# Kernel tuning notes

Measured on AMD Instinct MI355X. Metric: run time of the kernel, lower is better.

Reference implementation:

```python
import jax, jax.numpy as jnp
import numpy as np

HID, INTER, DK = 768, 1536, 128
NEG_INF = 1.0e12
LOG512 = float(np.log(512.0))


def setup_inputs() -> dict:
    key = jax.random.key(0)
    k1, k2, k3 = jax.random.split(key, 3)
    B, S = 4, 2048
    hidden_states = jax.random.normal(k1, (B, S, HID), dtype=jnp.float32)
    attention_mask = jnp.ones((B, S), dtype=jnp.int32)
    # i_dense: hidden -> 2*INTER + DK (no bias); o_dense: INTER -> hidden (no bias)
    Wi = jax.random.normal(k2, (HID, 2 * INTER + DK), dtype=jnp.float32) * (HID ** -0.5)
    Wo = jax.random.normal(k3, (INTER, HID), dtype=jnp.float32) * (INTER ** -0.5)
    q_gamma = jnp.ones((DK,), dtype=jnp.float32)  # ScaleOffset scale, offset=False
    k_gamma = jnp.ones((DK,), dtype=jnp.float32)
    return {"hidden_states": hidden_states, "Wi": Wi, "Wo": Wo,
            "q_gamma": q_gamma, "k_gamma": k_gamma,
            "attention_mask": attention_mask}


def reference(hidden_states, Wi, Wo, q_gamma, k_gamma, attention_mask):
    # i_dense + swish, then split into u, v, qk
    x = jax.nn.silu(jnp.einsum('bsh,ho->bso', hidden_states, Wi))
    u = x[..., :INTER]
    v = x[..., INTER:2 * INTER]
    qk = x[..., 2 * INTER:]
    q = qk * q_gamma
    k = qk * k_gamma
    # single-head attention scores
    a = jnp.einsum('bmd,bnd->bmn', q, k) / (DK ** 0.5)
    mask = attention_mask[:, None, :]  # [B,1,N]
    a = jnp.where(mask == 0, -NEG_INF, a)
    l = jnp.sum(attention_mask, axis=-1, keepdims=True)[:, :, None].astype(a.dtype)  # [B,1,1]
    # softmax_plus: softmax(a * log(l) / log(512))
    A = jax.nn.softmax(a * jnp.log(l) / LOG512, axis=-1)
    # dropout inactive in eval mode
    o = jnp.einsum('bmi,ih->bmh', u * jnp.einsum('bmn,bnd->bmd', A, v), Wo)
    return o
```

## Files before the change

### kernel.cpp

```cpp
#include <hip/hip_runtime.h>
#include <hip/hip_bf16.h>
#include <math.h>

#define BATCH 4
#define SEQ   2048
#define HID   768
#define INTER 1536
#define DK    128
#define NTOT  3200
#define MROWS 8192
#define LN512 6.2383246250395075f

typedef _Float16 half8  __attribute__((ext_vector_type(8)));
typedef float    floatx4 __attribute__((ext_vector_type(4)));

typedef const __attribute__((address_space(1))) unsigned int* gas1_t;
typedef __attribute__((address_space(3))) unsigned int* las3_t;

static __device__ __forceinline__ void load16(const _Float16* g, _Float16* l) {
    __builtin_amdgcn_global_load_lds((gas1_t)g, (las3_t)l, 16, 0, 0);
}
#define WAIT_VM(N)    asm volatile("s_waitcnt vmcnt(" #N ")" ::: "memory")
#define WAIT_LGKM0()  asm volatile("s_waitcnt lgkmcnt(0)" ::: "memory")
#define BARRIER_RAW() asm volatile("s_barrier" ::: "memory")

__global__ void cast_h_kernel(const float* __restrict__ in, _Float16* __restrict__ out, int n) {
    int i = (blockIdx.x * blockDim.x + threadIdx.x) * 8;
    if (i < n) {
        float4 a = *reinterpret_cast<const float4*>(in + i);
        float4 b = *reinterpret_cast<const float4*>(in + i + 4);
        half8 h = {(_Float16)a.x, (_Float16)a.y, (_Float16)a.z, (_Float16)a.w,
                   (_Float16)b.x, (_Float16)b.y, (_Float16)b.z, (_Float16)b.w};
        *reinterpret_cast<half8*>(out + i) = h;
    }
}

__global__ void trans_wi_kernel(const float* __restrict__ Wi, _Float16* __restrict__ WiT) {
    __shared__ _Float16 tile[32][33];
    const int c0 = blockIdx.x * 32, r0 = blockIdx.y * 32;
    const int tx = threadIdx.x, ty = threadIdx.y;
#pragma unroll
    for (int j = 0; j < 32; j += 8)
        tile[tx][ty + j] = (_Float16)Wi[(size_t)(r0 + ty + j) * NTOT + c0 + tx];
    __syncthreads();
#pragma unroll
    for (int j = 0; j < 32; j += 8)
        WiT[(size_t)(c0 + ty + j) * HID + r0 + tx] = tile[ty + j][tx];
}

__global__ void trans_wo_kernel(const float* __restrict__ Wo, _Float16* __restrict__ WoT) {
    __shared__ _Float16 tile[32][33];
    const int c0 = blockIdx.x * 32, r0 = blockIdx.y * 32;
    const int tx = threadIdx.x, ty = threadIdx.y;
#pragma unroll
    for (int j = 0; j < 32; j += 8)
        tile[tx][ty + j] = (_Float16)Wo[(size_t)(r0 + ty + j) * HID + c0 + tx];
    __syncthreads();
#pragma unroll
    for (int j = 0; j < 32; j += 8)
        WoT[(size_t)(c0 + ty + j) * INTER + r0 + tx] = tile[ty + j][tx];
}

__global__ void mask_scales_kernel(const int* __restrict__ mask, float* __restrict__ scales) {
    __shared__ int sh[256];
    int b = blockIdx.x;
    int s = 0;
    for (int i = threadIdx.x; i < SEQ; i += 256) s += mask[b * SEQ + i];
    sh[threadIdx.x] = s;
    __syncthreads();
    for (int off = 128; off > 0; off >>= 1) {
        if (threadIdx.x < off) sh[threadIdx.x] += sh[threadIdx.x + off];
        __syncthreads();
    }
    if (threadIdx.x == 0) scales[b] = logf((float)sh[0]) / LN512;
}

struct TileCtx {
    int tid, wave, lane, quad, l16, wm, wn, c0, c1, sw;
};
static __device__ __forceinline__ TileCtx make_ctx() {
    TileCtx t;
    t.tid = threadIdx.x;
    t.wave = t.tid >> 6; t.lane = t.tid & 63;
    t.quad = t.lane >> 4; t.l16 = t.lane & 15;
    t.wm = (t.wave & 1) * 64;
    t.wn = (t.wave >> 1) * 64;
    t.c0 = t.tid;
    t.c1 = t.tid + 256;
    t.sw = (t.l16 >> 1) & 3;
    return t;
}

static __device__ __forceinline__ void gemm_mainloop_db(
    const TileCtx& t,
    const _Float16* __restrict__ Ag, int lda,
    const _Float16* __restrict__ Bg, int ldb,
    int K, _Float16* smem, floatx4 acc[4][4])
{
    const int ar0 = t.c0 >> 2, ak0 = ((t.c0 & 3) ^ ((t.c0 >> 3) & 3)) * 8;
    const int ar1 = t.c1 >> 2, ak1 = ((t.c1 & 3) ^ ((t.c1 >> 3) & 3)) * 8;
    const _Float16* a0 = Ag + (size_t)ar0 * lda + ak0;
    const _Float16* a1 = Ag + (size_t)ar1 * lda + ak1;
    const _Float16* b0 = Bg + (size_t)ar0 * ldb + ak0;
    const _Float16* b1 = Bg + (size_t)ar1 * ldb + ak1;
    _Float16* Asl = smem + t.c0 * 8;
    _Float16* Bsl = smem + 8192 + t.c0 * 8;

    const int qsw = (t.quad ^ t.sw) * 8;

    load16(a0, Asl);
    load16(a1, Asl + 2048);
    load16(b0, Bsl);
    load16(b1, Bsl + 2048);

    int buf = 0;
    for (int k0 = 0; k0 < K; k0 += 32) {
        if (k0 + 32 < K) {
            const int nb = (buf ^ 1) * 4096;
            load16(a0 + k0 + 32, Asl + nb);
            load16(a1 + k0 + 32, Asl + nb + 2048);
            load16(b0 + k0 + 32, Bsl + nb);
            load16(b1 + k0 + 32, Bsl + nb + 2048);
            WAIT_VM(4);
        } else {
            WAIT_VM(0);
        }
        BARRIER_RAW();
        const _Float16* Ab = smem + buf * 4096;
        const _Float16* Bb = smem + 8192 + buf * 4096;
        half8 af[4], bf[4];
#pragma unroll
        for (int mt = 0; mt < 4; ++mt)
            af[mt] = *reinterpret_cast<const half8*>(Ab + (t.wm + mt * 16 + t.l16) * 32 + qsw);
#pragma unroll
        for (int nt = 0; nt < 4; ++nt)
            bf[nt] = *reinterpret_cast<const half8*>(Bb + (t.wn + nt * 16 + t.l16) * 32 + qsw);
#pragma unroll
        for (int mt = 0; mt < 4; ++mt)
#pragma unroll
            for (int nt = 0; nt < 4; ++nt)
                acc[mt][nt] = __builtin_amdgcn_mfma_f32_16x16x32_f16(af[mt], bf[nt], acc[mt][nt], 0, 0, 0);
        WAIT_LGKM0();
        BARRIER_RAW();
        buf ^= 1;
    }
}

__global__ __launch_bounds__(256) void gemm1_kernel(
    const _Float16* __restrict__ Hb, const _Float16* __restrict__ WiT,
    const float* __restrict__ qg, const float* __restrict__ kg,
    _Float16* __restrict__ u, _Float16* __restrict__ vT,
    _Float16* __restrict__ q, _Float16* __restrict__ k)
{
    __shared__ _Float16 smem[16384];
    TileCtx t = make_ctx();
    const int f = blockIdx.x;
    const int xcd = f & 7, i = f >> 3;
    const int m0 = ((xcd << 3) | (i & 7)) * 128;
    const int n0 = (i >> 3) * 128;

    floatx4 acc[4][4] = {};
    gemm_mainloop_db(t, Hb + (size_t)m0 * HID, HID, WiT + (size_t)n0 * HID, HID, HID, smem, acc);

    if (n0 >= INTER && n0 < 2 * INTER) {
        const int bb = m0 >> 11, sloc = m0 & (SEQ - 1), cI = n0 - INTER;
#pragma unroll
        for (int mt = 0; mt < 4; ++mt) {
#pragma unroll
            for (int nt = 0; nt < 4; ++nt) {
                int c = t.wn + nt * 16 + t.l16;
#pragma unroll
                for (int i2 = 0; i2 < 4; ++i2) {
                    int r = t.wm + mt * 16 + t.quad * 4 + i2;
                    float x = acc[mt][nt][i2];
                    float y = x / (1.0f + __expf(-x));
                    smem[c * 128 + (r ^ ((c & 15) << 3))] = (_Float16)y;
                }
            }
        }
        __syncthreads();
#pragma unroll
        for (int p = 0; p < 8; ++p) {
            int chunk = t.tid + p * 256;
            int cl = chunk >> 4, sc = chunk & 15;
            int scs = sc ^ (cl & 15);
            half8 v = *reinterpret_cast<const half8*>(smem + cl * 128 + scs * 8);
            *reinterpret_cast<half8*>(vT + ((size_t)bb * INTER + cI + cl) * SEQ + sloc + sc * 8) = v;
        }
    } else {
#pragma unroll
        for (int mt = 0; mt < 4; ++mt) {
#pragma unroll
            for (int nt = 0; nt < 4; ++nt) {
                int col = n0 + t.wn + nt * 16 + t.l16;
#pragma unroll
                for (int i2 = 0; i2 < 4; ++i2) {
                    int row = m0 + t.wm + mt * 16 + t.quad * 4 + i2;
                    float x = acc[mt][nt][i2];
                    float y = x / (1.0f + __expf(-x));
                    if (n0 < INTER) {
                        u[(size_t)row * INTER + col] = (_Float16)y;
                    } else {
                        int c = col - 2 * INTER;
                        q[(size_t)row * DK + c] = (_Float16)(y * qg[c]);
                        k[(size_t)row * DK + c] = (_Float16)(y * kg[c]);
                    }
                }
            }
        }
    }
}

__global__ __launch_bounds__(256) void scores_kernel(
    const _Float16* __restrict__ q, const _Float16* __restrict__ k,
    const int* __restrict__ mask, const float* __restrict__ scales,
    _Float16* __restrict__ P)
{
    const int b = blockIdx.y;
    const int m0 = blockIdx.x * 16;
    const int tid = threadIdx.x;
    const int wave = tid >> 6, lane = tid & 63, quad = lane >> 4, l16 = lane & 15;
    const float scale = scales[b];

    half8 aq[4];
    const _Float16* qrow = q + (b * SEQ + m0 + l16) * DK + quad * 8;
#pragma unroll
    for (int kk = 0; kk < 4; ++kk) aq[kk] = *reinterpret_cast<const half8*>(qrow + kk * 32);

    floatx4 sc[32];
#pragma unroll
    for (int nt = 0; nt < 32; ++nt) {
        int n0 = nt * 64 + wave * 16;
        const _Float16* krow = k + (b * SEQ + n0 + l16) * DK + quad * 8;
        floatx4 acc = {};
#pragma unroll
        for (int kk = 0; kk < 4; ++kk) {
            half8 bq = *reinterpret_cast<const half8*>(krow + kk * 32);
            acc = __builtin_amdgcn_mfma_f32_16x16x32_f16(aq[kk], bq, acc, 0, 0, 0);
        }
        sc[nt] = acc;
    }

    const float rs = 0.08838834764831845f * scale;
    const float mval = -1e12f * scale;
    float rmax[4] = {-3.4e38f, -3.4e38f, -3.4e38f, -3.4e38f};
#pragma unroll
    for (int nt = 0; nt < 32; ++nt) {
        int ncol = nt * 64 + wave * 16 + l16;
        bool mok = mask[b * SEQ + ncol] != 0;
#pragma unroll
        for (int i = 0; i < 4; ++i) {
            float s = mok ? sc[nt][i] * rs : mval;
            sc[nt][i] = s;
            rmax[i] = fmaxf(rmax[i], s);
        }
    }
#pragma unroll
    for (int i = 0; i < 4; ++i) {
#pragma unroll
        for (int off = 1; off < 16; off <<= 1)
            rmax[i] = fmaxf(rmax[i], __shfl_xor(rmax[i], off, 64));
    }
    __shared__ float redmax[4][16];
    __shared__ float redsum[4][16];
    if (l16 == 0) {
#pragma unroll
        for (int i = 0; i < 4; ++i) redmax[wave][quad * 4 + i] = rmax[i];
    }
    __syncthreads();
#pragma unroll
    for (int i = 0; i < 4; ++i) {
        int r = quad * 4 + i;
        rmax[i] = fmaxf(fmaxf(redmax[0][r], redmax[1][r]), fmaxf(redmax[2][r], redmax[3][r]));
    }
    float rsum[4] = {0.f, 0.f, 0.f, 0.f};
#pragma unroll
    for (int nt = 0; nt < 32; ++nt) {
#pragma unroll
        for (int i = 0; i < 4; ++i) {
            float e = __expf(sc[nt][i] - rmax[i]);
            sc[nt][i] = e;
            rsum[i] += e;
        }
    }
#pragma unroll
    for (int i = 0; i < 4; ++i) {
#pragma unroll
        for (int off = 1; off < 16; off <<= 1) rsum[i] += __shfl_xor(rsum[i], off, 64);
    }
    if (l16 == 0) {
#pragma unroll
        for (int i = 0; i < 4; ++i) redsum[wave][quad * 4 + i] = rsum[i];
    }
    __syncthreads();
#pragma unroll
    for (int i = 0; i < 4; ++i) {
        int r = quad * 4 + i;
        float tot = redsum[0][r] + redsum[1][r] + redsum[2][r] + redsum[3][r];
        float inv = 1.0f / tot;
        int row = m0 + r;
        _Float16* Prow = P + ((size_t)b * SEQ + row) * SEQ;
#pragma unroll
        for (int nt = 0; nt < 32; ++nt) {
            int ncol = nt * 64 + wave * 16 + l16;
            Prow[ncol] = (_Float16)(sc[nt][i] * inv);
        }
    }
}

__global__ __launch_bounds__(256) void pv_kernel(
    const _Float16* __restrict__ P, const _Float16* __restrict__ vT,
    _Float16* __restrict__ u)
{
    __shared__ _Float16 smem[16384];
    TileCtx t = make_ctx();
    const int f = blockIdx.x;
    const int xcd = f & 7, i = f >> 3;
    const int b = i / 24, j = i % 24;
    const int m0 = (xcd * 2 + (j & 1)) * 128;
    const int n0 = (j >> 1) * 128;
    const _Float16* Pb  = P  + (size_t)b * SEQ * SEQ;
    const _Float16* vTb = vT + (size_t)b * INTER * SEQ;

    floatx4 acc[4][4] = {};
    gemm_mainloop_db(t, Pb + (size_t)m0 * SEQ, SEQ, vTb + (size_t)n0 * SEQ, SEQ, SEQ, smem, acc);

#pragma unroll
    for (int mt = 0; mt < 4; ++mt) {
#pragma unroll
        for (int nt = 0; nt < 4; ++nt) {
            int col = n0 + t.wn + nt * 16 + t.l16;
#pragma unroll
            for (int i2 = 0; i2 < 4; ++i2) {
                int row = m0 + t.wm + mt * 16 + t.quad * 4 + i2;
                size_t gidx = ((size_t)(b * SEQ + row)) * INTER + col;
                float uv = (float)u[gidx];
                u[gidx] = (_Float16)(acc[mt][nt][i2] * uv);
            }
        }
    }
}

__global__ __launch_bounds__(256) void gemm2_kernel(
    const _Float16* __restrict__ tin, const _Float16* __restrict__ WoT,
    float* __restrict__ out)
{
    __shared__ _Float16 smem[16384];
    TileCtx t = make_ctx();
    const int f = blockIdx.x;
    const int xcd = f & 7, i = f >> 3;
    const int m0 = ((xcd << 3) | (i & 7)) * 128;
    const int n0 = (i >> 3) * 128;

    floatx4 acc[4][4] = {};
    gemm_mainloop_db(t, tin + (size_t)m0 * INTER, INTER, WoT + (size_t)n0 * INTER, INTER, INTER, smem, acc);

#pragma unroll
    for (int mt = 0; mt < 4; ++mt) {
#pragma unroll
        for (int nt = 0; nt < 4; ++nt) {
            int col = n0 + t.wn + nt * 16 + t.l16;
#pragma unroll
            for (int i2 = 0; i2 < 4; ++i2) {
                int row = m0 + t.wm + mt * 16 + t.quad * 4 + i2;
                out[(size_t)row * HID + col] = acc[mt][nt][i2];
            }
        }
    }
}

extern "C" void kernel_launch(void* const* d_in, const int* in_sizes, int n_in,
                              void* d_out, int out_size, void* d_ws, size_t ws_size,
                              hipStream_t stream) {
    const float* H    = (const float*)d_in[0];
    const float* Wi   = (const float*)d_in[1];
    const float* Wo   = (const float*)d_in[2];
    const float* qg   = (const float*)d_in[3];
    const float* kg   = (const float*)d_in[4];
    const int*   mask = (const int*)d_in[5];
    float* out = (float*)d_out;

    char* base = (char*)d_ws;
    size_t off = 0;
    auto alloc = [&](size_t bytes) { void* p = base + off; off = (off + bytes + 255) & ~(size_t)255; return p; };
    _Float16* Hb   = (_Float16*)alloc((size_t)MROWS * HID * 2);
    _Float16* WiT  = (_Float16*)alloc((size_t)NTOT * HID * 2);
    _Float16* WoT  = (_Float16*)alloc((size_t)HID * INTER * 2);
    _Float16* u    = (_Float16*)alloc((size_t)MROWS * INTER * 2);
    _Float16* vT   = (_Float16*)alloc((size_t)BATCH * INTER * SEQ * 2);
    _Float16* q    = (_Float16*)alloc((size_t)MROWS * DK * 2);
    _Float16* k    = (_Float16*)alloc((size_t)MROWS * DK * 2);
    _Float16* P    = (_Float16*)alloc((size_t)BATCH * SEQ * SEQ * 2);
    float*    scales = (float*)alloc(4 * sizeof(float));

    {
        int n = MROWS * HID;
        cast_h_kernel<<<n / 8 / 256, 256, 0, stream>>>(H, Hb, n);
        trans_wi_kernel<<<dim3(NTOT / 32, HID / 32), dim3(32, 8), 0, stream>>>(Wi, WiT);
        trans_wo_kernel<<<dim3(HID / 32, INTER / 32), dim3(32, 8), 0, stream>>>(Wo, WoT);
        mask_scales_kernel<<<BATCH, 256, 0, stream>>>(mask, scales);
    }
    gemm1_kernel<<<1600, 256, 0, stream>>>(Hb, WiT, qg, kg, u, vT, q, k);
    {
        dim3 grid(SEQ / 16, BATCH);
        scores_kernel<<<grid, 256, 0, stream>>>(q, k, mask, scales, P);
    }
    pv_kernel<<<768, 256, 0, stream>>>(P, vT, u);
    gemm2_kernel<<<384, 256, 0, stream>>>(u, WoT, out);
}
```

Baseline: 323.7 us.

## Switch GEMM main loop to three-stage LDS pipeline with one barrier

Measured after the change: 310.8 us. 4.0% less time.

```diff
diff --git a/kernel.cpp b/kernel.cpp
--- a/kernel.cpp
+++ b/kernel.cpp
@@ -91,7 +91,7 @@
     return t;
 }
 
-static __device__ __forceinline__ void gemm_mainloop_db(
+static __device__ __forceinline__ void gemm_mainloop_3s(
     const TileCtx& t,
     const _Float16* __restrict__ Ag, int lda,
     const _Float16* __restrict__ Bg, int ldb,
@@ -104,30 +104,35 @@
     const _Float16* b0 = Bg + (size_t)ar0 * ldb + ak0;
     const _Float16* b1 = Bg + (size_t)ar1 * ldb + ak1;
     _Float16* Asl = smem + t.c0 * 8;
-    _Float16* Bsl = smem + 8192 + t.c0 * 8;
+    _Float16* Bsl = smem + 12288 + t.c0 * 8;
+    const int nIter = K >> 5;
 
     const int qsw = (t.quad ^ t.sw) * 8;
 
-    load16(a0, Asl);
-    load16(a1, Asl + 2048);
-    load16(b0, Bsl);
-    load16(b1, Bsl + 2048);
-
-    int buf = 0;
-    for (int k0 = 0; k0 < K; k0 += 32) {
-        if (k0 + 32 < K) {
-            const int nb = (buf ^ 1) * 4096;
-            load16(a0 + k0 + 32, Asl + nb);
-            load16(a1 + k0 + 32, Asl + nb + 2048);
-            load16(b0 + k0 + 32, Bsl + nb);
-            load16(b1 + k0 + 32, Bsl + nb + 2048);
+    load16(a0, Asl);        load16(a1, Asl + 2048);
+    load16(b0, Bsl);        load16(b1, Bsl + 2048);
+    if (nIter > 1) {
+        load16(a0 + 32, Asl + 4096); load16(a1 + 32, Asl + 6144);
+        load16(b0 + 32, Bsl + 4096); load16(b1 + 32, Bsl + 6144);
+    }
+
+    int sc = 0;
+    int sp = 2;
+    for (int k = 0; k < nIter; ++k) {
+        if (k + 1 < nIter) {
             WAIT_VM(4);
         } else {
             WAIT_VM(0);
         }
         BARRIER_RAW();
-        const _Float16* Ab = smem + buf * 4096;
-        const _Float16* Bb = smem + 8192 + buf * 4096;
+        if (k + 2 < nIter) {
+            const int off = sp * 4096;
+            const int k0 = (k + 2) << 5;
+            load16(a0 + k0, Asl + off); load16(a1 + k0, Asl + off + 2048);
+            load16(b0 + k0, Bsl + off); load16(b1 + k0, Bsl + off + 2048);
+        }
+        const _Float16* Ab = smem + sc * 4096;
+        const _Float16* Bb = smem + 12288 + sc * 4096;
         half8 af[4], bf[4];
 #pragma unroll
         for (int mt = 0; mt < 4; ++mt)
@@ -141,8 +146,8 @@
             for (int nt = 0; nt < 4; ++nt)
                 acc[mt][nt] = __builtin_amdgcn_mfma_f32_16x16x32_f16(af[mt], bf[nt], acc[mt][nt], 0, 0, 0);
         WAIT_LGKM0();
-        BARRIER_RAW();
-        buf ^= 1;
+        sc = (sc == 2) ? 0 : sc + 1;
+        sp = (sp == 2) ? 0 : sp + 1;
     }
 }
 
@@ -152,7 +157,7 @@
     _Float16* __restrict__ u, _Float16* __restrict__ vT,
     _Float16* __restrict__ q, _Float16* __restrict__ k)
 {
-    __shared__ _Float16 smem[16384];
+    __shared__ _Float16 smem[24576];
     TileCtx t = make_ctx();
     const int f = blockIdx.x;
     const int xcd = f & 7, i = f >> 3;
@@ -160,9 +165,10 @@
     const int n0 = (i >> 3) * 128;
 
     floatx4 acc[4][4] = {};
-    gemm_mainloop_db(t, Hb + (size_t)m0 * HID, HID, WiT + (size_t)n0 * HID, HID, HID, smem, acc);
+    gemm_mainloop_3s(t, Hb + (size_t)m0 * HID, HID, WiT + (size_t)n0 * HID, HID, HID, smem, acc);
 
     if (n0 >= INTER && n0 < 2 * INTER) {
+        __syncthreads();
         const int bb = m0 >> 11, sloc = m0 & (SEQ - 1), cI = n0 - INTER;
 #pragma unroll
         for (int mt = 0; mt < 4; ++mt) {
@@ -312,7 +318,7 @@
     const _Float16* __restrict__ P, const _Float16* __restrict__ vT,
     _Float16* __restrict__ u)
 {
-    __shared__ _Float16 smem[16384];
+    __shared__ _Float16 smem[24576];
     TileCtx t = make_ctx();
     const int f = blockIdx.x;
     const int xcd = f & 7, i = f >> 3;
@@ -323,7 +329,7 @@
     const _Float16* vTb = vT + (size_t)b * INTER * SEQ;
 
     floatx4 acc[4][4] = {};
-    gemm_mainloop_db(t, Pb + (size_t)m0 * SEQ, SEQ, vTb + (size_t)n0 * SEQ, SEQ, SEQ, smem, acc);
+    gemm_mainloop_3s(t, Pb + (size_t)m0 * SEQ, SEQ, vTb + (size_t)n0 * SEQ, SEQ, SEQ, smem, acc);
 
 #pragma unroll
     for (int mt = 0; mt < 4; ++mt) {
@@ -345,7 +351,7 @@
     const _Float16* __restrict__ tin, const _Float16* __restrict__ WoT,
     float* __restrict__ out)
 {
-    __shared__ _Float16 smem[16384];
+    __shared__ _Float16 smem[24576];
     TileCtx t = make_ctx();
     const int f = blockIdx.x;
     const int xcd = f & 7, i = f >> 3;
@@ -353,7 +359,7 @@
     const int n0 = (i >> 3) * 128;
 
     floatx4 acc[4][4] = {};
-    gemm_mainloop_db(t, tin + (size_t)m0 * INTER, INTER, WoT + (size_t)n0 * INTER, INTER, INTER, smem, acc);
+    gemm_mainloop_3s(t, tin + (size_t)m0 * INTER, INTER, WoT + (size_t)n0 * INTER, INTER, INTER, smem, acc);
 
 #pragma unroll
     for (int mt = 0; mt < 4; ++mt) {
```
